# Optimization experiments

Hardware: AMD Instinct MI355X
Metric: run time of the kernel (lower is better)

The kernel has to match this reference:

```python
import jax, jax.numpy as jnp
import numpy as np

DIM, HEADS, RANK = 768, 12, 64
HEAD_DIM = DIM // HEADS

def _xavier(key, shape):
    fan_in, fan_out = shape[1], shape[0]
    std = (2.0 / (fan_in + fan_out)) ** 0.5
    return std * jax.random.normal(key, shape, dtype=jnp.float32)

def setup_inputs() -> dict:
    key = jax.random.key(0)
    ks = jax.random.split(key, 12)
    B, N = 8, 1024
    x = jax.random.normal(ks[0], (B, N, DIM), dtype=jnp.float32)
    params = {}
    for i, nm in enumerate(['Q', 'K', 'V']):
        params[f'W_{nm}0'] = _xavier(ks[1 + 3 * i], (DIM, RANK))
        params[f'W_{nm}1'] = _xavier(ks[2 + 3 * i], (HEADS, RANK))
        params[f'W_{nm}2'] = _xavier(ks[3 + 3 * i], (HEAD_DIM, RANK))
    proj_w = _xavier(ks[10], (DIM, DIM))
    proj_b = jnp.zeros((DIM,), dtype=jnp.float32)
    return dict(x=x, W_Q0=params['W_Q0'], W_Q1=params['W_Q1'], W_Q2=params['W_Q2'],
                W_K0=params['W_K0'], W_K1=params['W_K1'], W_K2=params['W_K2'],
                W_V0=params['W_V0'], W_V1=params['W_V1'], W_V2=params['W_V2'],
                proj_w=proj_w, proj_b=proj_b)

def _cp_proj(xh, W2, W1, W0, B, N, H, hd):
    # xh: [B,N,H,hd]; contract head_dim with W2 and heads with W1 -> [B,N,R], then expand to dim via W0
    t = jnp.einsum('blnd,dr,nr->blr', xh, W2, W1)
    out = jnp.einsum('blr,mr->blm', t, W0)          # [B,N,dim]
    return out.reshape(B, N, H, hd).transpose(0, 2, 1, 3)  # [B,H,N,hd]

def reference(x, W_Q0, W_Q1, W_Q2, W_K0, W_K1, W_K2, W_V0, W_V1, W_V2, proj_w, proj_b):
    B, N, C = x.shape
    H = W_Q1.shape[0]
    hd = C // H
    scale = hd ** -0.5
    xh = x.reshape(B, N, H, hd)
    q = _cp_proj(xh, W_Q2, W_Q1, W_Q0, B, N, H, hd)
    k = _cp_proj(xh, W_K2, W_K1, W_K0, B, N, H, hd)
    v = _cp_proj(xh, W_V2, W_V1, W_V0, B, N, H, hd)
    attn = jax.nn.softmax(jnp.einsum('bhqd,bhkd->bhqk', q, k) * scale, axis=-1)
    out = jnp.einsum('bhqk,bhkd->bhqd', attn, v).transpose(0, 2, 1, 3).reshape(B, N, C)
    return out @ proj_w.T + proj_b
```

## Files before the change

kernel.cpp:

```cpp
#include <hip/hip_runtime.h>

typedef unsigned short u16;
typedef __attribute__((ext_vector_type(8))) short bf16x8;
typedef __attribute__((ext_vector_type(4))) float f32x4;
typedef __attribute__((ext_vector_type(4))) unsigned short u16x4;
typedef __attribute__((ext_vector_type(8))) unsigned short u16x8;

#define AS1 __attribute__((address_space(1)))
#define AS3 __attribute__((address_space(3)))

__device__ __forceinline__ float b2f(u16 s) {
    return __uint_as_float(((unsigned)s) << 16);
}
__device__ __forceinline__ u16 f2b(float f) {
    unsigned u = __float_as_uint(f);
    unsigned r = 0x7fffu + ((u >> 16) & 1u);
    return (u16)((u + r) >> 16);
}

__device__ __forceinline__ unsigned packtrunc(float p0, float p1) {
#if __has_builtin(__builtin_amdgcn_perm)
    return __builtin_amdgcn_perm(__float_as_uint(p1), __float_as_uint(p0), 0x07060302u);
#else
    return (__float_as_uint(p0) >> 16) | (__float_as_uint(p1) & 0xffff0000u);
#endif
}

__device__ __forceinline__ void g2l16(const u16* g, u16* l) {
    __builtin_amdgcn_global_load_lds((const AS1 void*)g, (AS3 void*)l, 16, 0, 0);
}

#if __has_builtin(__builtin_amdgcn_exp2f)
#define EXP2(x) __builtin_amdgcn_exp2f(x)
#else
#define EXP2(x) exp2f(x)
#endif

__global__ __launch_bounds__(256) void build_small(
    const float* __restrict__ Wq0, const float* __restrict__ Wq1, const float* __restrict__ Wq2,
    const float* __restrict__ Wk0, const float* __restrict__ Wk1, const float* __restrict__ Wk2,
    const float* __restrict__ Wv0, const float* __restrict__ Wv1, const float* __restrict__ Wv2,
    const float* __restrict__ PW,
    u16* __restrict__ G, u16* __restrict__ W0b, u16* __restrict__ pwb)
{
    const int idx = blockIdx.x * 256 + threadIdx.x;
    if (idx < 147456) {
        const int row = idx / 768, c = idx - row * 768;
        const int which = row >> 6, r = row & 63;
        const int h = c >> 6, d = c & 63;
        const float* W1 = (which == 0) ? Wq1 : (which == 1) ? Wk1 : Wv1;
        const float* W2 = (which == 0) ? Wq2 : (which == 1) ? Wk2 : Wv2;
        G[idx] = f2b(W1[h * 64 + r] * W2[d * 64 + r]);
    } else if (idx < 294912) {
        const int j = idx - 147456;
        const int row = j >> 6, r = j & 63;
        const int which = row / 768, mm = row - which * 768;
        const float* W0 = (which == 0) ? Wq0 : (which == 1) ? Wk0 : Wv0;
        const float scale = (which == 0) ? 0.125f * 1.4426950408889634f : 1.0f;
        W0b[j] = f2b(W0[mm * 64 + r] * scale);
    } else {
        const int j = idx - 294912;
        const float4 v = ((const float4*)PW)[j];
        u16x4 o;
        o.x = f2b(v.x); o.y = f2b(v.y); o.z = f2b(v.z); o.w = f2b(v.w);
        ((u16x4*)pwb)[j] = o;
    }
}

__global__ __launch_bounds__(256, 2) void gemm_t(
    const float* __restrict__ X, const u16* __restrict__ G, u16* __restrict__ T)
{
    __shared__ u16 As[64 * 32];
    __shared__ u16 Bs[64 * 32];

    const int tid = threadIdx.x;
    const int lane = tid & 63, wv = tid >> 6;
    const int l15 = lane & 15, quad = lane >> 4;
    const int rowBase = blockIdx.y * 64;
    const int colBase = blockIdx.x * 64;

    const int srow = tid >> 2;
    const int scol = (tid & 3) * 8;
    const float* aS = X + (size_t)(rowBase + srow) * 768 + scol;
    const u16*  bS  = G + (size_t)(colBase + srow) * 768 + scol;

    float4 a0 = *(const float4*)(aS);
    float4 a1 = *(const float4*)(aS + 4);
    int4   b0 = *(const int4*)(bS);

    const f32x4 zero4 = {0.f, 0.f, 0.f, 0.f};
    f32x4 acc[4];
#pragma unroll
    for (int tn = 0; tn < 4; ++tn) acc[tn] = zero4;

    for (int kk = 0; kk < 768; kk += 32) {
        __syncthreads();
        u16x8 ap;
        ap[0] = f2b(a0.x); ap[1] = f2b(a0.y); ap[2] = f2b(a0.z); ap[3] = f2b(a0.w);
        ap[4] = f2b(a1.x); ap[5] = f2b(a1.y); ap[6] = f2b(a1.z); ap[7] = f2b(a1.w);
        *(u16x8*)&As[srow * 32 + scol] = ap;
        *(int4*)&Bs[srow * 32 + scol]  = b0;
        __syncthreads();

        if (kk < 736) {
            a0 = *(const float4*)(aS + kk + 32);
            a1 = *(const float4*)(aS + kk + 36);
            b0 = *(const int4*)(bS + kk + 32);
        }

        const bf16x8 af = *(const bf16x8*)(As + (wv * 16 + l15) * 32 + quad * 8);
#pragma unroll
        for (int tn = 0; tn < 4; ++tn) {
            const bf16x8 bf = *(const bf16x8*)(Bs + (tn * 16 + l15) * 32 + quad * 8);
            acc[tn] = __builtin_amdgcn_mfma_f32_16x16x32_bf16(af, bf, acc[tn], 0, 0, 0);
        }
    }

#pragma unroll
    for (int tn = 0; tn < 4; ++tn) {
        const int col = colBase + tn * 16 + l15;
#pragma unroll
        for (int r = 0; r < 4; ++r) {
            const int grow = rowBase + wv * 16 + quad * 4 + r;
            T[(size_t)grow * 192 + col] = f2b(acc[tn][r]);
        }
    }
}

__global__ __launch_bounds__(256, 2) void gemm_expand(
    const u16* __restrict__ T, const u16* __restrict__ W0b, u16* __restrict__ qkvp)
{
    __shared__ u16 As[128 * 32];
    __shared__ u16 Bs[128 * 32];

    const int tid  = threadIdx.x;
    const int lane = tid & 63, wv = tid >> 6;
    const int l15  = lane & 15, quad = lane >> 4;
    const int rowBase = blockIdx.y * 128;
    const int colBase = blockIdx.x * 128;
    const int which = blockIdx.x / 6;

    const int srow = wv * 32 + (lane >> 2);
    const int scol = (lane & 3) * 8;
    const u16* aSrc = T   + (size_t)(rowBase + srow) * 192 + which * 64 + scol;
    const u16* bSrc = W0b + (size_t)(colBase + srow) * 64 + scol;
    u16* aDst = As + wv * 1024;
    u16* bDst = Bs + wv * 1024;

    const f32x4 zero4 = {0.f, 0.f, 0.f, 0.f};
    f32x4 acc[4][4];
#pragma unroll
    for (int tm = 0; tm < 4; ++tm)
#pragma unroll
        for (int tn = 0; tn < 4; ++tn) acc[tm][tn] = zero4;

    const int wr = (wv >> 1) * 64, wc = (wv & 1) * 64;

    for (int kk = 0; kk < 64; kk += 32) {
        __syncthreads();
        g2l16(aSrc + kk,            aDst);
        g2l16(aSrc + kk + 16 * 192, aDst + 512);
        g2l16(bSrc + kk,            bDst);
        g2l16(bSrc + kk + 16 * 64,  bDst + 512);
        __syncthreads();

        bf16x8 af[4], bfm[4];
#pragma unroll
        for (int t = 0; t < 4; ++t) {
            af[t]  = *(const bf16x8*)(As + (wr + t * 16 + l15) * 32 + quad * 8);
            bfm[t] = *(const bf16x8*)(Bs + (wc + t * 16 + l15) * 32 + quad * 8);
        }
#pragma unroll
        for (int tm = 0; tm < 4; ++tm)
#pragma unroll
            for (int tn = 0; tn < 4; ++tn)
                acc[tm][tn] = __builtin_amdgcn_mfma_f32_16x16x32_bf16(
                    af[tm], bfm[tn], acc[tm][tn], 0, 0, 0);
    }

    const int mmBase = colBase - which * 768 + wc;
    if (which < 2) {
        u16* outp = qkvp + (size_t)which * 6291456;
#pragma unroll
        for (int tm = 0; tm < 4; ++tm) {
            const int grow = rowBase + wr + tm * 16 + quad * 4;
            const int b = grow >> 10, l = grow & 1023;
#pragma unroll
            for (int tn = 0; tn < 4; ++tn) {
                const int mmv = mmBase + tn * 16 + l15;
                const int h = mmv >> 6, d = mmv & 63;
                const size_t base = (((size_t)(b * 12 + h) * 1024 + l) << 6) + d;
#pragma unroll
                for (int r = 0; r < 4; ++r)
                    outp[base + (size_t)r * 64] = f2b(acc[tm][tn][r]);
            }
        }
    } else {
        u16* outp = qkvp + (size_t)2 * 6291456;
#pragma unroll
        for (int tm = 0; tm < 4; ++tm) {
            const int grow = rowBase + wr + tm * 16 + quad * 4;
            const int b = grow >> 10, l = grow & 1023;
#pragma unroll
            for (int tn = 0; tn < 4; ++tn) {
                const int mmv = mmBase + tn * 16 + l15;
                const int h = mmv >> 6, d = mmv & 63;
                u16x4 pk;
                pk.x = f2b(acc[tm][tn][0]); pk.y = f2b(acc[tm][tn][1]);
                pk.z = f2b(acc[tm][tn][2]); pk.w = f2b(acc[tm][tn][3]);
                *(u16x4*)(outp + (((size_t)(b * 12 + h) * 64 + d) << 10) + l) = pk;
            }
        }
    }
}

__global__ __launch_bounds__(256, 3) void flash_attn5(
    const u16* __restrict__ qkv, u16* __restrict__ o)
{
    const int qt = blockIdx.x;
    const int bh = blockIdx.y;
    const int b = bh / 12, h = bh - b * 12;
    const u16* qp = qkv + (size_t)bh * 65536 + qt * 8192;
    const u16* kp = qkv + 6291456 + (size_t)bh * 65536;
    const u16* vp = qkv + 2 * 6291456 + (size_t)bh * 65536;

    __shared__ u16 Ks[64][72];
    __shared__ u16 Vs[64][72];

    const int t = threadIdx.x;
    const int lane = t & 63, wv = t >> 6;
    const int l15 = lane & 15, quad = lane >> 4;

    bf16x8 qf[2][2];
#pragma unroll
    for (int qg = 0; qg < 2; ++qg) {
        qf[qg][0] = *(const bf16x8*)(qp + (wv * 32 + qg * 16 + l15) * 64 + quad * 8);
        qf[qg][1] = *(const bf16x8*)(qp + (wv * 32 + qg * 16 + l15) * 64 + 32 + quad * 8);
    }

    const int srow = t >> 2;
    const int scol = (t & 3) * 16;
    const int p5 = srow & 31;
    const int lrow = (srow & 32) | ((p5 & 4) << 2) | ((p5 & 16) >> 1)
                   | ((p5 & 8) >> 1) | (p5 & 3);

    bf16x8 vone = {};
    if (l15 == 0) {
#pragma unroll
        for (int j = 0; j < 8; ++j) vone[j] = (short)0x3F80;
    }

    int4 kr0 = *(const int4*)(kp + srow * 64 + scol);
    int4 kr1 = *(const int4*)(kp + srow * 64 + scol + 8);
    int4 vr0 = *(const int4*)(vp + srow * 1024 + scol);
    int4 vr1 = *(const int4*)(vp + srow * 1024 + scol + 8);

    const f32x4 zero4 = {0.f, 0.f, 0.f, 0.f};
    f32x4 o_acc[2][4];
    f32x4 Lacc[2] = {zero4, zero4};
#pragma unroll
    for (int qg = 0; qg < 2; ++qg)
#pragma unroll
        for (int tn = 0; tn < 4; ++tn) o_acc[qg][tn] = zero4;

    for (int kt = 0; kt < 16; ++kt) {
        __syncthreads();
        *(int4*)&Ks[lrow][scol]     = kr0;
        *(int4*)&Ks[lrow][scol + 8] = kr1;
        *(int4*)&Vs[srow][scol]     = vr0;
        *(int4*)&Vs[srow][scol + 8] = vr1;
        __syncthreads();

        if (kt < 15) {
            kr0 = *(const int4*)(kp + (kt + 1) * 4096 + srow * 64 + scol);
            kr1 = *(const int4*)(kp + (kt + 1) * 4096 + srow * 64 + scol + 8);
            vr0 = *(const int4*)(vp + srow * 1024 + (kt + 1) * 64 + scol);
            vr1 = *(const int4*)(vp + srow * 1024 + (kt + 1) * 64 + scol + 8);
        }

        f32x4 Sacc[2][4];
#pragma unroll
        for (int qg = 0; qg < 2; ++qg)
#pragma unroll
            for (int tk = 0; tk < 4; ++tk) Sacc[qg][tk] = zero4;
#pragma unroll
        for (int ks = 0; ks < 2; ++ks) {
#pragma unroll
            for (int tk = 0; tk < 4; ++tk) {
                const bf16x8 kf = *(const bf16x8*)&Ks[tk * 16 + l15][ks * 32 + quad * 8];
                Sacc[0][tk] = __builtin_amdgcn_mfma_f32_16x16x32_bf16(kf, qf[0][ks], Sacc[0][tk], 0, 0, 0);
                Sacc[1][tk] = __builtin_amdgcn_mfma_f32_16x16x32_bf16(kf, qf[1][ks], Sacc[1][tk], 0, 0, 0);
            }
        }

        union { bf16x8 v; unsigned u[4]; } pf[2][2];
#pragma unroll
        for (int qg = 0; qg < 2; ++qg)
#pragma unroll
            for (int tk = 0; tk < 4; ++tk) {
                const float p0 = EXP2(Sacc[qg][tk][0]);
                const float p1 = EXP2(Sacc[qg][tk][1]);
                const float p2 = EXP2(Sacc[qg][tk][2]);
                const float p3 = EXP2(Sacc[qg][tk][3]);
                const int g = tk >> 1, hf = (tk & 1) * 2;
                pf[qg][g].u[hf + 0] = packtrunc(p0, p1);
                pf[qg][g].u[hf + 1] = packtrunc(p2, p3);
            }

#pragma unroll
        for (int g = 0; g < 2; ++g) {
#pragma unroll
            for (int tn = 0; tn < 4; ++tn) {
                const bf16x8 vf = *(const bf16x8*)&Vs[tn * 16 + l15][g * 32 + quad * 8];
                o_acc[0][tn] = __builtin_amdgcn_mfma_f32_16x16x32_bf16(pf[0][g].v, vf, o_acc[0][tn], 0, 0, 0);
                o_acc[1][tn] = __builtin_amdgcn_mfma_f32_16x16x32_bf16(pf[1][g].v, vf, o_acc[1][tn], 0, 0, 0);
            }
            Lacc[0] = __builtin_amdgcn_mfma_f32_16x16x32_bf16(pf[0][g].v, vone, Lacc[0], 0, 0, 0);
            Lacc[1] = __builtin_amdgcn_mfma_f32_16x16x32_bf16(pf[1][g].v, vone, Lacc[1], 0, 0, 0);
        }
    }

#pragma unroll
    for (int qg = 0; qg < 2; ++qg) {
#pragma unroll
        for (int r = 0; r < 4; ++r) {
            const float Lv = __shfl(Lacc[qg][r], quad << 4, 64);
            const float inv = 1.0f / Lv;
            const int token = qt * 128 + wv * 32 + qg * 16 + quad * 4 + r;
#pragma unroll
            for (int tn = 0; tn < 4; ++tn) {
                const int col = h * 64 + tn * 16 + l15;
                o[(size_t)(b * 1024 + token) * 768 + col] = f2b(o_acc[qg][tn][r] * inv);
            }
        }
    }
}

__global__ __launch_bounds__(256, 2) void gemm_proj(
    const u16* __restrict__ A, const u16* __restrict__ Bt,
    float* __restrict__ C, const float* __restrict__ bias)
{
    __shared__ u16 As[128 * 32];
    __shared__ u16 Bs[128 * 32];

    const int tid  = threadIdx.x;
    const int lane = tid & 63, wv = tid >> 6;
    const int l15  = lane & 15, quad = lane >> 4;
    const int rowBase = blockIdx.y * 128;
    const int colBase = blockIdx.x * 128;

    const int srow = wv * 32 + (lane >> 2);
    const int scol = (lane & 3) * 8;
    const u16* aSrc = A  + (size_t)(rowBase + srow) * 768 + scol;
    const u16* bSrc = Bt + (size_t)(colBase + srow) * 768 + scol;
    u16* aDst = As + wv * 1024;
    u16* bDst = Bs + wv * 1024;

    const f32x4 zero4 = {0.f, 0.f, 0.f, 0.f};
    f32x4 acc[4][4];
#pragma unroll
    for (int tm = 0; tm < 4; ++tm)
#pragma unroll
        for (int tn = 0; tn < 4; ++tn) acc[tm][tn] = zero4;

    const int wr = (wv >> 1) * 64, wc = (wv & 1) * 64;

    for (int kk = 0; kk < 768; kk += 32) {
        __syncthreads();
        g2l16(aSrc + kk,            aDst);
        g2l16(aSrc + kk + 16 * 768, aDst + 512);
        g2l16(bSrc + kk,            bDst);
        g2l16(bSrc + kk + 16 * 768, bDst + 512);
        __syncthreads();

        bf16x8 af[4], bfm[4];
#pragma unroll
        for (int t = 0; t < 4; ++t) {
            af[t]  = *(const bf16x8*)(As + (wr + t * 16 + l15) * 32 + quad * 8);
            bfm[t] = *(const bf16x8*)(Bs + (wc + t * 16 + l15) * 32 + quad * 8);
        }
#pragma unroll
        for (int tm = 0; tm < 4; ++tm)
#pragma unroll
            for (int tn = 0; tn < 4; ++tn)
                acc[tm][tn] = __builtin_amdgcn_mfma_f32_16x16x32_bf16(
                    af[tm], bfm[tn], acc[tm][tn], 0, 0, 0);
    }

#pragma unroll
    for (int tm = 0; tm < 4; ++tm) {
        const int grow = rowBase + wr + tm * 16 + quad * 4;
#pragma unroll
        for (int tn = 0; tn < 4; ++tn) {
            const int gcol = colBase + wc + tn * 16 + l15;
            const float bv = bias[gcol];
#pragma unroll
            for (int r = 0; r < 4; ++r)
                C[(size_t)(grow + r) * 768 + gcol] = acc[tm][tn][r] + bv;
        }
    }
}

extern "C" void kernel_launch(void* const* d_in, const int* in_sizes, int n_in,
                              void* d_out, int out_size, void* d_ws, size_t ws_size,
                              hipStream_t stream)
{
    const float* x      = (const float*)d_in[0];
    const float* Wq0    = (const float*)d_in[1];
    const float* Wq1    = (const float*)d_in[2];
    const float* Wq2    = (const float*)d_in[3];
    const float* Wk0    = (const float*)d_in[4];
    const float* Wk1    = (const float*)d_in[5];
    const float* Wk2    = (const float*)d_in[6];
    const float* Wv0    = (const float*)d_in[7];
    const float* Wv1    = (const float*)d_in[8];
    const float* Wv2    = (const float*)d_in[9];
    const float* proj_w = (const float*)d_in[10];
    const float* proj_b = (const float*)d_in[11];
    float* outp = (float*)d_out;

    char* ws = (char*)d_ws;
    u16* T    = (u16*)ws;
    u16* G    = (u16*)(ws + 3145728);
    u16* W0b  = (u16*)(ws + 3440640);
    u16* pwb  = (u16*)(ws + 3735552);
    u16* attn = (u16*)(ws + 4915200);
    u16* qkv  = (u16*)(ws + 17498112);

    build_small<<<1728, 256, 0, stream>>>(Wq0, Wq1, Wq2, Wk0, Wk1, Wk2, Wv0, Wv1, Wv2,
                                          proj_w, G, W0b, pwb);
    gemm_t<<<dim3(3, 128), 256, 0, stream>>>(x, G, T);
    gemm_expand<<<dim3(18, 64), 256, 0, stream>>>(T, W0b, qkv);
    flash_attn5<<<dim3(8, 96), 256, 0, stream>>>(qkv, attn);
    gemm_proj<<<dim3(6, 64), 256, 0, stream>>>(attn, pwb, outp, proj_b);
}
```

Baseline: 185.9 us.

## Fold V expansion into output projection via low-rank V and precomputed W0·Wproj

Instead of expanding V to full head dim, attention now runs over the rank-64 V factor (tvt, written transposed by gemm_t). Each head's V expansion matrix is folded into the output projection weights (Dcat = proj_w per head times Wv0), computed in the prep kernel. This removes the V part of gemm_expand and its 12.6MB write/read. gemm_out is retiled to 128x64 with three blocks per CU. Folding the weights in bf16 changes rounding slightly.

```diff
diff --git a/kernel.cpp b/kernel.cpp
--- a/kernel.cpp
+++ b/kernel.cpp
@@ -36,39 +36,62 @@
 #define EXP2(x) exp2f(x)
 #endif
 
-__global__ __launch_bounds__(256) void build_small(
+__global__ __launch_bounds__(256) void build_prep(
     const float* __restrict__ Wq0, const float* __restrict__ Wq1, const float* __restrict__ Wq2,
     const float* __restrict__ Wk0, const float* __restrict__ Wk1, const float* __restrict__ Wk2,
     const float* __restrict__ Wv0, const float* __restrict__ Wv1, const float* __restrict__ Wv2,
     const float* __restrict__ PW,
-    u16* __restrict__ G, u16* __restrict__ W0b, u16* __restrict__ pwb)
-{
-    const int idx = blockIdx.x * 256 + threadIdx.x;
-    if (idx < 147456) {
-        const int row = idx / 768, c = idx - row * 768;
-        const int which = row >> 6, r = row & 63;
-        const int h = c >> 6, d = c & 63;
-        const float* W1 = (which == 0) ? Wq1 : (which == 1) ? Wk1 : Wv1;
-        const float* W2 = (which == 0) ? Wq2 : (which == 1) ? Wk2 : Wv2;
-        G[idx] = f2b(W1[h * 64 + r] * W2[d * 64 + r]);
-    } else if (idx < 294912) {
-        const int j = idx - 147456;
-        const int row = j >> 6, r = j & 63;
-        const int which = row / 768, mm = row - which * 768;
-        const float* W0 = (which == 0) ? Wq0 : (which == 1) ? Wk0 : Wv0;
-        const float scale = (which == 0) ? 0.125f * 1.4426950408889634f : 1.0f;
-        W0b[j] = f2b(W0[mm * 64 + r] * scale);
+    u16* __restrict__ G, u16* __restrict__ W0b, u16* __restrict__ Dcat)
+{
+    const int bx = blockIdx.x;
+    const int t = threadIdx.x;
+    if (bx < 1152) {
+        const int idx = bx * 256 + t;
+        if (idx < 147456) {
+            const int row = idx / 768, c = idx - row * 768;
+            const int which = row >> 6, r = row & 63;
+            const int h = c >> 6, d = c & 63;
+            const float* W1 = (which == 0) ? Wq1 : (which == 1) ? Wk1 : Wv1;
+            const float* W2 = (which == 0) ? Wq2 : (which == 1) ? Wk2 : Wv2;
+            G[idx] = f2b(W1[h * 64 + r] * W2[d * 64 + r]);
+        } else {
+            const int j = idx - 147456;
+            const int row = j >> 6, r = j & 63;
+            const int which = row / 768, mm = row - which * 768;
+            const float* W0 = (which == 0) ? Wq0 : (which == 1) ? Wk0 : Wv0;
+            const float scale = (which == 0) ? 0.125f * 1.4426950408889634f : 1.0f;
+            W0b[j] = f2b(W0[mm * 64 + r] * scale);
+        }
     } else {
-        const int j = idx - 294912;
-        const float4 v = ((const float4*)PW)[j];
-        u16x4 o;
-        o.x = f2b(v.x); o.y = f2b(v.y); o.z = f2b(v.z); o.w = f2b(v.w);
-        ((u16x4*)pwb)[j] = o;
+        __shared__ float w0s[64 * 65];
+        __shared__ float pws[32 * 65];
+        const int hb = bx - 1152;
+        const int h = hb / 24, mBase = (hb - h * 24) * 32;
+        for (int i = t; i < 4096; i += 256) {
+            const int d = i >> 6, r = i & 63;
+            w0s[d * 65 + r] = Wv0[(h * 64 + d) * 64 + r];
+        }
+        for (int i = t; i < 2048; i += 256) {
+            const int mi = i >> 6, d = i & 63;
+            pws[mi * 65 + d] = PW[(size_t)(mBase + mi) * 768 + h * 64 + d];
+        }
+        __syncthreads();
+        const int r = t & 63, mi0 = t >> 6;
+        float w0c[64];
+#pragma unroll
+        for (int d = 0; d < 64; ++d) w0c[d] = w0s[d * 65 + r];
+        for (int mi = mi0; mi < 32; mi += 4) {
+            float acc = 0.f;
+#pragma unroll
+            for (int d = 0; d < 64; ++d) acc += pws[mi * 65 + d] * w0c[d];
+            Dcat[(size_t)(mBase + mi) * 768 + h * 64 + r] = f2b(acc);
+        }
     }
 }
 
 __global__ __launch_bounds__(256, 2) void gemm_t(
-    const float* __restrict__ X, const u16* __restrict__ G, u16* __restrict__ T)
+    const float* __restrict__ X, const u16* __restrict__ G,
+    u16* __restrict__ T, u16* __restrict__ tvt)
 {
     __shared__ u16 As[64 * 32];
     __shared__ u16 Bs[64 * 32];
@@ -116,19 +139,31 @@
         }
     }
 
-#pragma unroll
-    for (int tn = 0; tn < 4; ++tn) {
-        const int col = colBase + tn * 16 + l15;
-#pragma unroll
-        for (int r = 0; r < 4; ++r) {
-            const int grow = rowBase + wv * 16 + quad * 4 + r;
-            T[(size_t)grow * 192 + col] = f2b(acc[tn][r]);
+    if (colBase < 128) {
+#pragma unroll
+        for (int tn = 0; tn < 4; ++tn) {
+            const int col = colBase + tn * 16 + l15;
+#pragma unroll
+            for (int r = 0; r < 4; ++r) {
+                const int grow = rowBase + wv * 16 + quad * 4 + r;
+                T[(size_t)grow * 128 + col] = f2b(acc[tn][r]);
+            }
+        }
+    } else {
+#pragma unroll
+        for (int tn = 0; tn < 4; ++tn) {
+            const int rr = tn * 16 + l15;
+            const int grow = rowBase + wv * 16 + quad * 4;
+            u16x4 pk;
+            pk.x = f2b(acc[tn][0]); pk.y = f2b(acc[tn][1]);
+            pk.z = f2b(acc[tn][2]); pk.w = f2b(acc[tn][3]);
+            *(u16x4*)(tvt + (size_t)rr * 8192 + grow) = pk;
         }
     }
 }
 
 __global__ __launch_bounds__(256, 2) void gemm_expand(
-    const u16* __restrict__ T, const u16* __restrict__ W0b, u16* __restrict__ qkvp)
+    const u16* __restrict__ T, const u16* __restrict__ W0b, u16* __restrict__ qkp)
 {
     __shared__ u16 As[128 * 32];
     __shared__ u16 Bs[128 * 32];
@@ -142,7 +177,7 @@
 
     const int srow = wv * 32 + (lane >> 2);
     const int scol = (lane & 3) * 8;
-    const u16* aSrc = T   + (size_t)(rowBase + srow) * 192 + which * 64 + scol;
+    const u16* aSrc = T   + (size_t)(rowBase + srow) * 128 + which * 64 + scol;
     const u16* bSrc = W0b + (size_t)(colBase + srow) * 64 + scol;
     u16* aDst = As + wv * 1024;
     u16* bDst = Bs + wv * 1024;
@@ -159,7 +194,7 @@
     for (int kk = 0; kk < 64; kk += 32) {
         __syncthreads();
         g2l16(aSrc + kk,            aDst);
-        g2l16(aSrc + kk + 16 * 192, aDst + 512);
+        g2l16(aSrc + kk + 16 * 128, aDst + 512);
         g2l16(bSrc + kk,            bDst);
         g2l16(bSrc + kk + 16 * 64,  bDst + 512);
         __syncthreads();
@@ -179,50 +214,32 @@
     }
 
     const int mmBase = colBase - which * 768 + wc;
-    if (which < 2) {
-        u16* outp = qkvp + (size_t)which * 6291456;
-#pragma unroll
-        for (int tm = 0; tm < 4; ++tm) {
-            const int grow = rowBase + wr + tm * 16 + quad * 4;
-            const int b = grow >> 10, l = grow & 1023;
-#pragma unroll
-            for (int tn = 0; tn < 4; ++tn) {
-                const int mmv = mmBase + tn * 16 + l15;
-                const int h = mmv >> 6, d = mmv & 63;
-                const size_t base = (((size_t)(b * 12 + h) * 1024 + l) << 6) + d;
-#pragma unroll
-                for (int r = 0; r < 4; ++r)
-                    outp[base + (size_t)r * 64] = f2b(acc[tm][tn][r]);
-            }
-        }
-    } else {
-        u16* outp = qkvp + (size_t)2 * 6291456;
-#pragma unroll
-        for (int tm = 0; tm < 4; ++tm) {
-            const int grow = rowBase + wr + tm * 16 + quad * 4;
-            const int b = grow >> 10, l = grow & 1023;
-#pragma unroll
-            for (int tn = 0; tn < 4; ++tn) {
-                const int mmv = mmBase + tn * 16 + l15;
-                const int h = mmv >> 6, d = mmv & 63;
-                u16x4 pk;
-                pk.x = f2b(acc[tm][tn][0]); pk.y = f2b(acc[tm][tn][1]);
-                pk.z = f2b(acc[tm][tn][2]); pk.w = f2b(acc[tm][tn][3]);
-                *(u16x4*)(outp + (((size_t)(b * 12 + h) * 64 + d) << 10) + l) = pk;
-            }
-        }
-    }
-}
-
-__global__ __launch_bounds__(256, 3) void flash_attn5(
-    const u16* __restrict__ qkv, u16* __restrict__ o)
+    u16* outp = qkp + (size_t)which * 6291456;
+#pragma unroll
+    for (int tm = 0; tm < 4; ++tm) {
+        const int grow = rowBase + wr + tm * 16 + quad * 4;
+        const int b = grow >> 10, l = grow & 1023;
+#pragma unroll
+        for (int tn = 0; tn < 4; ++tn) {
+            const int mmv = mmBase + tn * 16 + l15;
+            const int h = mmv >> 6, d = mmv & 63;
+            const size_t base = (((size_t)(b * 12 + h) * 1024 + l) << 6) + d;
+#pragma unroll
+            for (int r = 0; r < 4; ++r)
+                outp[base + (size_t)r * 64] = f2b(acc[tm][tn][r]);
+        }
+    }
+}
+
+__global__ __launch_bounds__(256, 3) void flash_attn6(
+    const u16* __restrict__ qk, const u16* __restrict__ tvt, u16* __restrict__ Z)
 {
     const int qt = blockIdx.x;
     const int bh = blockIdx.y;
     const int b = bh / 12, h = bh - b * 12;
-    const u16* qp = qkv + (size_t)bh * 65536 + qt * 8192;
-    const u16* kp = qkv + 6291456 + (size_t)bh * 65536;
-    const u16* vp = qkv + 2 * 6291456 + (size_t)bh * 65536;
+    const u16* qp = qk + (size_t)bh * 65536 + qt * 8192;
+    const u16* kp = qk + 6291456 + (size_t)bh * 65536;
+    const u16* vp = tvt + b * 1024;
 
     __shared__ u16 Ks[64][72];
     __shared__ u16 Vs[64][72];
@@ -252,8 +269,8 @@
 
     int4 kr0 = *(const int4*)(kp + srow * 64 + scol);
     int4 kr1 = *(const int4*)(kp + srow * 64 + scol + 8);
-    int4 vr0 = *(const int4*)(vp + srow * 1024 + scol);
-    int4 vr1 = *(const int4*)(vp + srow * 1024 + scol + 8);
+    int4 vr0 = *(const int4*)(vp + (size_t)srow * 8192 + scol);
+    int4 vr1 = *(const int4*)(vp + (size_t)srow * 8192 + scol + 8);
 
     const f32x4 zero4 = {0.f, 0.f, 0.f, 0.f};
     f32x4 o_acc[2][4];
@@ -274,8 +291,8 @@
         if (kt < 15) {
             kr0 = *(const int4*)(kp + (kt + 1) * 4096 + srow * 64 + scol);
             kr1 = *(const int4*)(kp + (kt + 1) * 4096 + srow * 64 + scol + 8);
-            vr0 = *(const int4*)(vp + srow * 1024 + (kt + 1) * 64 + scol);
-            vr1 = *(const int4*)(vp + srow * 1024 + (kt + 1) * 64 + scol + 8);
+            vr0 = *(const int4*)(vp + (size_t)srow * 8192 + (kt + 1) * 64 + scol);
+            vr1 = *(const int4*)(vp + (size_t)srow * 8192 + (kt + 1) * 64 + scol + 8);
         }
 
         f32x4 Sacc[2][4];
@@ -330,57 +347,56 @@
 #pragma unroll
             for (int tn = 0; tn < 4; ++tn) {
                 const int col = h * 64 + tn * 16 + l15;
-                o[(size_t)(b * 1024 + token) * 768 + col] = f2b(o_acc[qg][tn][r] * inv);
+                Z[(size_t)(b * 1024 + token) * 768 + col] = f2b(o_acc[qg][tn][r] * inv);
             }
         }
     }
 }
 
-__global__ __launch_bounds__(256, 2) void gemm_proj(
+__global__ __launch_bounds__(256, 3) void gemm_out(
     const u16* __restrict__ A, const u16* __restrict__ Bt,
     float* __restrict__ C, const float* __restrict__ bias)
 {
     __shared__ u16 As[128 * 32];
-    __shared__ u16 Bs[128 * 32];
+    __shared__ u16 Bs[64 * 32];
 
     const int tid  = threadIdx.x;
     const int lane = tid & 63, wv = tid >> 6;
     const int l15  = lane & 15, quad = lane >> 4;
     const int rowBase = blockIdx.y * 128;
-    const int colBase = blockIdx.x * 128;
-
-    const int srow = wv * 32 + (lane >> 2);
-    const int scol = (lane & 3) * 8;
-    const u16* aSrc = A  + (size_t)(rowBase + srow) * 768 + scol;
-    const u16* bSrc = Bt + (size_t)(colBase + srow) * 768 + scol;
+    const int colBase = blockIdx.x * 64;
+
+    const int srowA = wv * 32 + (lane >> 2);
+    const int srowB = wv * 16 + (lane >> 2);
+    const int scol  = (lane & 3) * 8;
+    const u16* aSrc = A  + (size_t)(rowBase + srowA) * 768 + scol;
+    const u16* bSrc = Bt + (size_t)(colBase + srowB) * 768 + scol;
     u16* aDst = As + wv * 1024;
-    u16* bDst = Bs + wv * 1024;
+    u16* bDst = Bs + wv * 512;
 
     const f32x4 zero4 = {0.f, 0.f, 0.f, 0.f};
-    f32x4 acc[4][4];
-#pragma unroll
-    for (int tm = 0; tm < 4; ++tm)
+    f32x4 acc[2][4];
+#pragma unroll
+    for (int tm = 0; tm < 2; ++tm)
 #pragma unroll
         for (int tn = 0; tn < 4; ++tn) acc[tm][tn] = zero4;
-
-    const int wr = (wv >> 1) * 64, wc = (wv & 1) * 64;
 
     for (int kk = 0; kk < 768; kk += 32) {
         __syncthreads();
         g2l16(aSrc + kk,            aDst);
         g2l16(aSrc + kk + 16 * 768, aDst + 512);
         g2l16(bSrc + kk,            bDst);
-        g2l16(bSrc + kk + 16 * 768, bDst + 512);
-        __syncthreads();
-
-        bf16x8 af[4], bfm[4];
-#pragma unroll
-        for (int t = 0; t < 4; ++t) {
-            af[t]  = *(const bf16x8*)(As + (wr + t * 16 + l15) * 32 + quad * 8);
-            bfm[t] = *(const bf16x8*)(Bs + (wc + t * 16 + l15) * 32 + quad * 8);
-        }
-#pragma unroll
-        for (int tm = 0; tm < 4; ++tm)
+        __syncthreads();
+
+        bf16x8 af[2], bfm[4];
+#pragma unroll
+        for (int t = 0; t < 2; ++t)
+            af[t]  = *(const bf16x8*)(As + (wv * 32 + t * 16 + l15) * 32 + quad * 8);
+#pragma unroll
+        for (int t = 0; t < 4; ++t)
+            bfm[t] = *(const bf16x8*)(Bs + (t * 16 + l15) * 32 + quad * 8);
+#pragma unroll
+        for (int tm = 0; tm < 2; ++tm)
 #pragma unroll
             for (int tn = 0; tn < 4; ++tn)
                 acc[tm][tn] = __builtin_amdgcn_mfma_f32_16x16x32_bf16(
@@ -388,11 +404,11 @@
     }
 
 #pragma unroll
-    for (int tm = 0; tm < 4; ++tm) {
-        const int grow = rowBase + wr + tm * 16 + quad * 4;
+    for (int tm = 0; tm < 2; ++tm) {
+        const int grow = rowBase + wv * 32 + tm * 16 + quad * 4;
 #pragma unroll
         for (int tn = 0; tn < 4; ++tn) {
-            const int gcol = colBase + wc + tn * 16 + l15;
+            const int gcol = colBase + tn * 16 + l15;
             const float bv = bias[gcol];
 #pragma unroll
             for (int r = 0; r < 4; ++r)
@@ -421,16 +437,17 @@
 
     char* ws = (char*)d_ws;
     u16* T    = (u16*)ws;
+    u16* tvt  = (u16*)(ws + 2097152);
     u16* G    = (u16*)(ws + 3145728);
     u16* W0b  = (u16*)(ws + 3440640);
-    u16* pwb  = (u16*)(ws + 3735552);
-    u16* attn = (u16*)(ws + 4915200);
-    u16* qkv  = (u16*)(ws + 17498112);
-
-    build_small<<<1728, 256, 0, stream>>>(Wq0, Wq1, Wq2, Wk0, Wk1, Wk2, Wv0, Wv1, Wv2,
-                                          proj_w, G, W0b, pwb);
-    gemm_t<<<dim3(3, 128), 256, 0, stream>>>(x, G, T);
-    gemm_expand<<<dim3(18, 64), 256, 0, stream>>>(T, W0b, qkv);
-    flash_attn5<<<dim3(8, 96), 256, 0, stream>>>(qkv, attn);
-    gemm_proj<<<dim3(6, 64), 256, 0, stream>>>(attn, pwb, outp, proj_b);
-}
+    u16* Dcat = (u16*)(ws + 3735552);
+    u16* Zcat = (u16*)(ws + 4915200);
+    u16* qk   = (u16*)(ws + 17498112);
+
+    build_prep<<<1440, 256, 0, stream>>>(Wq0, Wq1, Wq2, Wk0, Wk1, Wk2, Wv0, Wv1, Wv2,
+                                         proj_w, G, W0b, Dcat);
+    gemm_t<<<dim3(3, 128), 256, 0, stream>>>(x, G, T, tvt);
+    gemm_expand<<<dim3(12, 64), 256, 0, stream>>>(T, W0b, qk);
+    flash_attn6<<<dim3(8, 96), 256, 0, stream>>>(qk, tvt, Zcat);
+    gemm_out<<<dim3(12, 64), 256, 0, stream>>>(Zcat, Dcat, outp, proj_b);
+}
```

New measurement: 180.1 us. -3.1%, faster.
